# Performance work log

Hardware: AMD Instinct MI355X
Metric: run time of the kernel (lower is better)

Reference implementation:

```python
import jax, jax.numpy as jnp
import numpy as np

B = 1048576
L = 4   # latent_dim
F = 4   # f_dim
H = 32  # hidden width


def setup_inputs() -> dict:
    key = jax.random.key(0)
    ks = jax.random.split(key, 10)
    z = jax.random.normal(ks[0], (B, L, F), jnp.float32)
    z_int = jax.random.normal(ks[1], (B, L, F), jnp.float32)
    mask = jax.random.randint(ks[2], (L, L), 0, 2, jnp.int32)
    I = jax.random.randint(ks[3], (B, 1, L), 0, 2, jnp.int32)
    W1 = jax.random.normal(ks[4], (L * F, H), jnp.float32) * (1.0 / np.sqrt(L * F))
    b1 = jnp.zeros((H,), jnp.float32)
    W2 = jax.random.normal(ks[5], (H, H), jnp.float32) * (1.0 / np.sqrt(H))
    b2 = jnp.zeros((H,), jnp.float32)
    W3 = jax.random.normal(ks[6], (H, F), jnp.float32) * (1.0 / np.sqrt(H))
    b3 = jnp.zeros((F,), jnp.float32)
    return dict(z=z, z_int=z_int, W1=W1, b1=b1, W2=W2, b2=b2, W3=W3, b3=b3,
                mask=mask, I=I)


def reference(z, z_int, W1, b1, W2, b2, W3, b3, mask, I):
    # NOTE: in the original torch code, the I-conditional writes are always
    # overwritten by the subsequent column assignment, so I and z_int do not
    # affect the output (dead code, faithfully reproduced).
    Bn = z.shape[0]
    maskf = mask.astype(z.dtype)
    cols = maskf.T                                   # [L, L], row i == mask[:, i]
    # (z * mask[:, i]) broadcasts mask[:, i] over z's LAST dim, as in torch.
    masked = (z[None, :, :, :] * cols[:, None, None, :]).reshape(L, Bn, L * F)
    h = jax.nn.relu(jnp.einsum('ibk,kh->ibh', masked, W1) + b1)
    h = jax.nn.relu(jnp.einsum('ibh,hm->ibm', h, W2) + b2)
    out_net = jnp.einsum('ibm,mf->ibf', h, W3) + b3  # [L, B, F]
    # one eps vector of shape [F] per column i, broadcast over batch
    eps = jax.random.normal(jax.random.key(42), (L, F), z.dtype)
    out_net = out_net + eps[:, None, :]
    cond = jnp.any(mask == 1, axis=0)                # [L]: `1 in mask[:, i]`
    zt = jnp.swapaxes(z, 0, 1)                       # [L, B, F]
    out = jnp.where(cond[:, None, None], out_net, zt)
    return jnp.swapaxes(out, 0, 1)                   # [B, L, F]
```

## Files before the change

kernel.cpp:

```cpp
#include <hip/hip_runtime.h>
#include <cmath>
#include <cstdint>
#include <cstring>


static inline uint32_t rotl32(uint32_t v, int r) { return (v << r) | (v >> (32 - r)); }

static void threefry2x32_42(uint32_t x0, uint32_t x1, uint32_t& o0, uint32_t& o1) {
    const uint32_t k0 = 0u, k1 = 42u;
    const uint32_t ks[3] = { k0, k1, k0 ^ k1 ^ 0x1BD11BDAu };
    static const int R[8] = { 13, 15, 26, 6, 17, 29, 16, 24 };
    x0 += ks[0];
    x1 += ks[1];
    for (int g = 1; g <= 5; ++g) {
        const int* rr = &R[((g - 1) & 1) * 4];
        for (int j = 0; j < 4; ++j) {
            x0 += x1;
            x1 = rotl32(x1, rr[j]);
            x1 ^= x0;
        }
        x0 += ks[g % 3];
        x1 += ks[(g + 1) % 3] + (uint32_t)g;
    }
    o0 = x0;
    o1 = x1;
}

static double erfinv_d(double x) {
    float xf = (float)x;
    float w = -logf((1.0f - xf) * (1.0f + xf));
    float p;
    if (w < 5.0f) {
        w -= 2.5f;
        p = 2.81022636e-08f;
        p = fmaf(p, w, 3.43273939e-07f);
        p = fmaf(p, w, -3.5233877e-06f);
        p = fmaf(p, w, -4.39150654e-06f);
        p = fmaf(p, w, 0.00021858087f);
        p = fmaf(p, w, -0.00125372503f);
        p = fmaf(p, w, -0.00417768164f);
        p = fmaf(p, w, 0.246640727f);
        p = fmaf(p, w, 1.50140941f);
    } else {
        w = sqrtf(w) - 3.0f;
        p = -0.000200214257f;
        p = fmaf(p, w, 0.000100950558f);
        p = fmaf(p, w, 0.00134934322f);
        p = fmaf(p, w, -0.00367342844f);
        p = fmaf(p, w, 0.00573950773f);
        p = fmaf(p, w, -0.0076224613f);
        p = fmaf(p, w, 0.00943887047f);
        p = fmaf(p, w, 1.00167406f);
        p = fmaf(p, w, 2.83297682f);
    }
    double y = (double)(p * xf);
    const double c = 1.1283791670955126;
    for (int it = 0; it < 3; ++it) {
        double err = erf(y) - x;
        y -= err / (c * exp(-y * y));
    }
    return y;
}

struct EpsT { float e[16]; };

static void compute_eps(float* e) {
    const float lo = -0.99999994f;
    for (int i = 0; i < 16; ++i) {
        uint32_t a, b;
        threefry2x32_42(0u, (uint32_t)i, a, b);
        uint32_t bits = a ^ b;
        uint32_t fb = (bits >> 9) | 0x3f800000u;
        float f;
        memcpy(&f, &fb, 4);
        float u = f - 1.0f;
        float v = u * 2.0f + lo;
        if (v < lo) v = lo;
        e[i] = (float)(sqrt(2.0) * erfinv_d((double)v));
    }
}


typedef _Float16 half8 __attribute__((ext_vector_type(8)));
typedef __fp16  fp16x2 __attribute__((ext_vector_type(2)));
typedef __fp16  fp16x4 __attribute__((ext_vector_type(4)));
typedef __fp16  fp16x8 __attribute__((ext_vector_type(8)));
typedef float floatx16 __attribute__((ext_vector_type(16)));

static __device__ inline half8 relu_pack8(float a0, float a1, float a2, float a3,
                                          float a4, float a5, float a6, float a7) {
    fp16x2 p0 = __builtin_amdgcn_cvt_pkrtz(fmaxf(a0, 0.f), fmaxf(a1, 0.f));
    fp16x2 p1 = __builtin_amdgcn_cvt_pkrtz(fmaxf(a2, 0.f), fmaxf(a3, 0.f));
    fp16x2 p2 = __builtin_amdgcn_cvt_pkrtz(fmaxf(a4, 0.f), fmaxf(a5, 0.f));
    fp16x2 p3 = __builtin_amdgcn_cvt_pkrtz(fmaxf(a6, 0.f), fmaxf(a7, 0.f));
    fp16x4 q0 = __builtin_shufflevector(p0, p1, 0, 1, 2, 3);
    fp16x4 q1 = __builtin_shufflevector(p2, p3, 0, 1, 2, 3);
    fp16x8 r  = __builtin_shufflevector(q0, q1, 0, 1, 2, 3, 4, 5, 6, 7);
    return __builtin_bit_cast(half8, r);
}

__global__ __launch_bounds__(256) void scm_mfma(
    const float* __restrict__ z,
    const float* __restrict__ W1, const float* __restrict__ b1,
    const float* __restrict__ W2, const float* __restrict__ b2,
    const float* __restrict__ W3, const float* __restrict__ b3,
    const int* __restrict__ mask,
    float* __restrict__ out, EpsT ep, int B)
{
    const int lane = threadIdx.x & 63;
    const int hv   = lane >> 5;
    const int n    = lane & 31;
    const int wid  = blockIdx.x * (blockDim.x >> 6) + (threadIdx.x >> 6);
    const int nw   = gridDim.x * (blockDim.x >> 6);
    const int T    = B >> 5;

    int mk[16];
#pragma unroll
    for (int t = 0; t < 16; ++t) mk[t] = mask[t];
    int cond[4];
#pragma unroll
    for (int i = 0; i < 4; ++i) cond[i] = mk[i] | mk[4 + i] | mk[8 + i] | mk[12 + i];

    half8 w1m[4], w2f[2], w3f[2];
#pragma unroll
    for (int j = 0; j < 8; ++j) {
        const int k = hv * 8 + j;
        const float w = W1[k * 32 + n];
#pragma unroll
        for (int i = 0; i < 4; ++i)
            w1m[i][j] = mk[(j & 3) * 4 + i] ? (_Float16)w : (_Float16)0.f;
    }
#pragma unroll
    for (int q = 0; q < 2; ++q)
#pragma unroll
        for (int j = 0; j < 8; ++j) {
            const int row = 16 * q + 4 * hv + 8 * (j >> 2) + (j & 3);
            w2f[q][j] = (_Float16)W2[row * 32 + n];
            w3f[q][j] = (n < 8) ? (_Float16)W3[row * 4 + (n & 3)] : (_Float16)0.f;
        }

    floatx16 b1v, b2v;
#pragma unroll
    for (int r = 0; r < 16; ++r) {
        const int h = (r & 3) + 8 * (r >> 2) + 4 * hv;
        b1v[r] = b1[h];
        b2v[r] = b2[h];
    }
    float eb[8];
#pragma unroll
    for (int s2 = 0; s2 < 2; ++s2)
#pragma unroll
        for (int f = 0; f < 4; ++f)
            eb[s2 * 4 + f] = b3[f] + ep.e[(2 * hv + s2) * 4 + f] - b2v[f];

    int t = wid;
    float4 za = make_float4(0.f, 0.f, 0.f, 0.f), zb = za;
    if (t < T) {
        const float4* p = reinterpret_cast<const float4*>(z + ((size_t)t * 32 + n) * 16) + hv * 2;
        za = p[0]; zb = p[1];
    }
    while (t < T) {
        const int tn = t + nw;
        float4 na = make_float4(0.f, 0.f, 0.f, 0.f), nb = na;
        if (tn < T) {
            const float4* p = reinterpret_cast<const float4*>(z + ((size_t)tn * 32 + n) * 16) + hv * 2;
            na = p[0]; nb = p[1];
        }

        const float zf[8] = { za.x, za.y, za.z, za.w, zb.x, zb.y, zb.z, zb.w };
        half8 bz;
#pragma unroll
        for (int j = 0; j < 8; ++j) bz[j] = (_Float16)zf[j];

        float ov[8];
#pragma unroll
        for (int u = 0; u < 8; ++u) ov[u] = zf[u];

#pragma unroll
        for (int i = 0; i < 4; ++i) {
            floatx16 c1 = __builtin_amdgcn_mfma_f32_32x32x16_f16(w1m[i], bz, b1v, 0, 0, 0);
            half8 pa = relu_pack8(c1[0], c1[1], c1[2], c1[3], c1[4], c1[5], c1[6], c1[7]);
            half8 pb = relu_pack8(c1[8], c1[9], c1[10], c1[11], c1[12], c1[13], c1[14], c1[15]);
            floatx16 c2 = __builtin_amdgcn_mfma_f32_32x32x16_f16(w2f[0], pa, b2v, 0, 0, 0);
            c2 = __builtin_amdgcn_mfma_f32_32x32x16_f16(w2f[1], pb, c2, 0, 0, 0);
            half8 qa = relu_pack8(c2[0], c2[1], c2[2], c2[3], c2[4], c2[5], c2[6], c2[7]);
            half8 qb = relu_pack8(c2[8], c2[9], c2[10], c2[11], c2[12], c2[13], c2[14], c2[15]);
            floatx16 c3 = __builtin_amdgcn_mfma_f32_32x32x16_f16(w3f[0], qa, b2v, 0, 0, 0);
            c3 = __builtin_amdgcn_mfma_f32_32x32x16_f16(w3f[1], qb, c3, 0, 0, 0);

            const int  s2 = i & 1;
            const bool ow = ((i >> 1) == hv);
            const bool wr = ow && (cond[i] != 0);
#pragma unroll
            for (int f = 0; f < 4; ++f) {
                const float vv = c3[f] + eb[s2 * 4 + f];
                ov[s2 * 4 + f] = wr ? vv : ov[s2 * 4 + f];
            }
        }

        float4* op = reinterpret_cast<float4*>(out + ((size_t)t * 32 + n) * 16 + hv * 8);
        op[0] = make_float4(ov[0], ov[1], ov[2], ov[3]);
        op[1] = make_float4(ov[4], ov[5], ov[6], ov[7]);

        t = tn; za = na; zb = nb;
    }
}

extern "C" void kernel_launch(void* const* d_in, const int* in_sizes, int n_in,
                              void* d_out, int out_size, void* d_ws, size_t ws_size,
                              hipStream_t stream) {
    const float* z  = (const float*)d_in[0];
    const float* W1 = (const float*)d_in[2];
    const float* b1 = (const float*)d_in[3];
    const float* W2 = (const float*)d_in[4];
    const float* b2 = (const float*)d_in[5];
    const float* W3 = (const float*)d_in[6];
    const float* b3 = (const float*)d_in[7];
    const int* mask = (const int*)d_in[8];
    float* out = (float*)d_out;

    const int B = in_sizes[0] / 16;

    EpsT ep;
    compute_eps(ep.e);

    dim3 grid(2048), block(256);
    hipLaunchKernelGGL(scm_mfma, grid, block, 0, stream,
                       z, W1, b1, W2, b2, W3, b3, mask, out, ep, B);
}
```

Measured before the change: 201.5 us.

## Cut register pressure with on-the-fly masked W1, nontemporal stores, smaller grid

Instead of keeping four pre-masked W1 fragments in registers, the kernel keeps one W1 fragment plus scalar uniform masks read via readfirstlane, and builds each masked fragment with bitwise ANDs inside the loop. It adds a launch_bounds occupancy hint of 4 blocks per SM, writes output with nontemporal stores to avoid cache pollution, and halves the grid to 1024 blocks. The aim is fewer VGPRs and higher occupancy. The cost is a few extra ALU ops per iteration, and the smaller grid gives each wave more serial work.

```diff
diff --git a/kernel.cpp b/kernel.cpp
--- a/kernel.cpp
+++ b/kernel.cpp
@@ -85,6 +85,8 @@
 typedef __fp16  fp16x2 __attribute__((ext_vector_type(2)));
 typedef __fp16  fp16x4 __attribute__((ext_vector_type(4)));
 typedef __fp16  fp16x8 __attribute__((ext_vector_type(8)));
+typedef uint32_t uint32x4 __attribute__((ext_vector_type(4)));
+typedef float floatx4 __attribute__((ext_vector_type(4)));
 typedef float floatx16 __attribute__((ext_vector_type(16)));
 
 static __device__ inline half8 relu_pack8(float a0, float a1, float a2, float a3,
@@ -99,7 +101,7 @@
     return __builtin_bit_cast(half8, r);
 }
 
-__global__ __launch_bounds__(256) void scm_mfma(
+__global__ __launch_bounds__(256, 4) void scm_mfma(
     const float* __restrict__ z,
     const float* __restrict__ W1, const float* __restrict__ b1,
     const float* __restrict__ W2, const float* __restrict__ b2,
@@ -114,22 +116,23 @@
     const int nw   = gridDim.x * (blockDim.x >> 6);
     const int T    = B >> 5;
 
-    int mk[16];
-#pragma unroll
-    for (int t = 0; t < 16; ++t) mk[t] = mask[t];
+    int mku[16];
+#pragma unroll
+    for (int t = 0; t < 16; ++t) mku[t] = __builtin_amdgcn_readfirstlane(mask[t]);
     int cond[4];
-#pragma unroll
-    for (int i = 0; i < 4; ++i) cond[i] = mk[i] | mk[4 + i] | mk[8 + i] | mk[12 + i];
-
-    half8 w1m[4], w2f[2], w3f[2];
-#pragma unroll
-    for (int j = 0; j < 8; ++j) {
-        const int k = hv * 8 + j;
-        const float w = W1[k * 32 + n];
-#pragma unroll
-        for (int i = 0; i < 4; ++i)
-            w1m[i][j] = mk[(j & 3) * 4 + i] ? (_Float16)w : (_Float16)0.f;
-    }
+    uint32_t M01[4], M23[4];
+#pragma unroll
+    for (int i = 0; i < 4; ++i) {
+        cond[i] = mku[i] | mku[4 + i] | mku[8 + i] | mku[12 + i];
+        M01[i] = (mku[i]      ? 0x0000FFFFu : 0u) | (mku[4 + i]  ? 0xFFFF0000u : 0u);
+        M23[i] = (mku[8 + i]  ? 0x0000FFFFu : 0u) | (mku[12 + i] ? 0xFFFF0000u : 0u);
+    }
+
+    half8 w1, w2f[2], w3f[2];
+#pragma unroll
+    for (int j = 0; j < 8; ++j)
+        w1[j] = (_Float16)W1[(hv * 8 + j) * 32 + n];
+    const uint32x4 w1u = __builtin_bit_cast(uint32x4, w1);
 #pragma unroll
     for (int q = 0; q < 2; ++q)
 #pragma unroll
@@ -154,31 +157,38 @@
             eb[s2 * 4 + f] = b3[f] + ep.e[(2 * hv + s2) * 4 + f] - b2v[f];
 
     int t = wid;
-    float4 za = make_float4(0.f, 0.f, 0.f, 0.f), zb = za;
+    floatx4 za = { 0.f, 0.f, 0.f, 0.f }, zb = za;
     if (t < T) {
-        const float4* p = reinterpret_cast<const float4*>(z + ((size_t)t * 32 + n) * 16) + hv * 2;
+        const floatx4* p = reinterpret_cast<const floatx4*>(z + ((size_t)t * 32 + n) * 16) + hv * 2;
         za = p[0]; zb = p[1];
     }
     while (t < T) {
         const int tn = t + nw;
-        float4 na = make_float4(0.f, 0.f, 0.f, 0.f), nb = na;
+        floatx4 na = { 0.f, 0.f, 0.f, 0.f }, nb = na;
         if (tn < T) {
-            const float4* p = reinterpret_cast<const float4*>(z + ((size_t)tn * 32 + n) * 16) + hv * 2;
+            const floatx4* p = reinterpret_cast<const floatx4*>(z + ((size_t)tn * 32 + n) * 16) + hv * 2;
             na = p[0]; nb = p[1];
         }
 
-        const float zf[8] = { za.x, za.y, za.z, za.w, zb.x, zb.y, zb.z, zb.w };
         half8 bz;
-#pragma unroll
-        for (int j = 0; j < 8; ++j) bz[j] = (_Float16)zf[j];
+        bz[0] = (_Float16)za.x; bz[1] = (_Float16)za.y;
+        bz[2] = (_Float16)za.z; bz[3] = (_Float16)za.w;
+        bz[4] = (_Float16)zb.x; bz[5] = (_Float16)zb.y;
+        bz[6] = (_Float16)zb.z; bz[7] = (_Float16)zb.w;
 
         float ov[8];
-#pragma unroll
-        for (int u = 0; u < 8; ++u) ov[u] = zf[u];
+        ov[0] = za.x; ov[1] = za.y; ov[2] = za.z; ov[3] = za.w;
+        ov[4] = zb.x; ov[5] = zb.y; ov[6] = zb.z; ov[7] = zb.w;
 
 #pragma unroll
         for (int i = 0; i < 4; ++i) {
-            floatx16 c1 = __builtin_amdgcn_mfma_f32_32x32x16_f16(w1m[i], bz, b1v, 0, 0, 0);
+            uint32x4 wm;
+            wm.x = w1u.x & M01[i];
+            wm.y = w1u.y & M23[i];
+            wm.z = w1u.z & M01[i];
+            wm.w = w1u.w & M23[i];
+            const half8 w1m = __builtin_bit_cast(half8, wm);
+            floatx16 c1 = __builtin_amdgcn_mfma_f32_32x32x16_f16(w1m, bz, b1v, 0, 0, 0);
             half8 pa = relu_pack8(c1[0], c1[1], c1[2], c1[3], c1[4], c1[5], c1[6], c1[7]);
             half8 pb = relu_pack8(c1[8], c1[9], c1[10], c1[11], c1[12], c1[13], c1[14], c1[15]);
             floatx16 c2 = __builtin_amdgcn_mfma_f32_32x32x16_f16(w2f[0], pa, b2v, 0, 0, 0);
@@ -198,9 +208,11 @@
             }
         }
 
-        float4* op = reinterpret_cast<float4*>(out + ((size_t)t * 32 + n) * 16 + hv * 8);
-        op[0] = make_float4(ov[0], ov[1], ov[2], ov[3]);
-        op[1] = make_float4(ov[4], ov[5], ov[6], ov[7]);
+        floatx4* op = reinterpret_cast<floatx4*>(out + ((size_t)t * 32 + n) * 16 + hv * 8);
+        floatx4 o0 = { ov[0], ov[1], ov[2], ov[3] };
+        floatx4 o1 = { ov[4], ov[5], ov[6], ov[7] };
+        __builtin_nontemporal_store(o0, op);
+        __builtin_nontemporal_store(o1, op + 1);
 
         t = tn; za = na; zb = nb;
     }
@@ -224,7 +236,7 @@
     EpsT ep;
     compute_eps(ep.e);
 
-    dim3 grid(2048), block(256);
+    dim3 grid(1024), block(256);
     hipLaunchKernelGGL(scm_mfma, grid, block, 0, stream,
                        z, W1, b1, W2, b2, W3, b3, mask, out, ep, B);
 }
```

After: 185.5 us. 1.09x faster.
